# Kernel tuning notes

Measured on AMD Instinct MI355X. Metric: run time of the kernel, lower is better.

Reference implementation:

```python
import jax, jax.numpy as jnp
import numpy as np

B, S, D, H, E = 2, 512, 768, 12, 8
FF = 4 * D
HD = D // H


def setup_inputs() -> dict:
    key = jax.random.key(0)
    ks = jax.random.split(key, 12)
    s = 0.02
    return {
        "x": jax.random.normal(ks[0], (B, S, D), jnp.float32),
        "ln1_g": jnp.ones((D,), jnp.float32),
        "ln1_b": jnp.zeros((D,), jnp.float32),
        "ln2_g": jnp.ones((D,), jnp.float32),
        "ln2_b": jnp.zeros((D,), jnp.float32),
        "in_proj_w": jax.random.normal(ks[1], (3 * D, D), jnp.float32) * s,
        "in_proj_b": jax.random.normal(ks[2], (3 * D,), jnp.float32) * s,
        "out_proj_w": jax.random.normal(ks[3], (D, D), jnp.float32) * s,
        "out_proj_b": jax.random.normal(ks[4], (D,), jnp.float32) * s,
        "router_w": jax.random.normal(ks[5], (E, D), jnp.float32) * s,
        "router_b": jax.random.normal(ks[6], (E,), jnp.float32) * s,
        "w1": jax.random.normal(ks[7], (E, D, FF), jnp.float32) * s,
        "b1": jax.random.normal(ks[8], (E, FF), jnp.float32) * s,
        "w2": jax.random.normal(ks[9], (E, FF, D), jnp.float32) * s,
        "b2": jax.random.normal(ks[10], (E, D), jnp.float32) * s,
    }


def _layernorm(x, g, b, eps=1e-5):
    mu = x.mean(-1, keepdims=True)
    var = ((x - mu) ** 2).mean(-1, keepdims=True)
    return (x - mu) * jax.lax.rsqrt(var + eps) * g + b


def _forward(x, ln1_g, ln1_b, ln2_g, ln2_b, in_proj_w, in_proj_b,
             out_proj_w, out_proj_b, router_w, router_b, w1, b1, w2, b2):
    # --- self-attention sublayer (pre-norm per torch module ordering) ---
    h = _layernorm(x, ln1_g, ln1_b)
    qkv = h @ in_proj_w.T + in_proj_b                     # [B,S,3D]
    q, k, v = jnp.split(qkv, 3, axis=-1)
    to_heads = lambda t: t.reshape(B, S, H, HD).transpose(0, 2, 1, 3)  # [B,H,S,hd]
    q, k, v = to_heads(q), to_heads(k), to_heads(v)
    scores = jnp.einsum('bhqd,bhkd->bhqk', q, k) / np.float32(np.sqrt(HD))
    attn = jax.nn.softmax(scores, axis=-1)
    o = jnp.einsum('bhqk,bhkd->bhqd', attn, v).transpose(0, 2, 1, 3).reshape(B, S, D)
    o = o @ out_proj_w.T + out_proj_b
    x = x + o
    # --- MoE sublayer: top-2 routing, renormalized gates ---
    h2 = _layernorm(x, ln2_g, ln2_b)
    t = h2.reshape(-1, D)                                  # [T,D]
    logits = t @ router_w.T + router_b                     # [T,E]
    probs = jax.nn.softmax(logits, axis=-1)
    top_v, top_i = jax.lax.top_k(probs, 2)                 # [T,2]
    top_v = top_v / top_v.sum(-1, keepdims=True)
    # per-(token, expert) combine weight (0 if expert not in token's top-2)
    comb = jnp.sum(jax.nn.one_hot(top_i, E, dtype=probs.dtype) * top_v[..., None], axis=1)  # [T,E]
    # dense grouped-FFN: every token through every expert, zero-weighted combine
    hid = jax.nn.gelu(jnp.einsum('td,edf->tef', t, w1) + b1, approximate=False)  # exact GELU as torch
    y = jnp.einsum('tef,efd->ted', hid, w2) + b2           # [T,E,D]
    moe = jnp.einsum('te,ted->td', comb, y).reshape(B, S, D)
    return x + moe


def reference(x, ln1_g, ln1_b, ln2_g, ln2_b, in_proj_w, in_proj_b,
              out_proj_w, out_proj_b, router_w, router_b, w1, b1, w2, b2):
    return _forward(x, ln1_g, ln1_b, ln2_g, ln2_b, in_proj_w, in_proj_b,
                    out_proj_w, out_proj_b, router_w, router_b, w1, b1, w2, b2)
```

## Files before the change

### kernel.cpp

```cpp
#include <hip/hip_runtime.h>
#include <hip/hip_bf16.h>

#define BATCH 2
#define SEQ 512
#define DIM 768
#define HEADS 12
#define NEXP 8
#define FFDIM 3072
#define HDIM 64
#define NTOK (BATCH*SEQ)
#define NENT (2*NTOK)

typedef __hip_bfloat16 bf16;
typedef __attribute__((ext_vector_type(8))) short s8v;
typedef __attribute__((ext_vector_type(4))) float f4v;

typedef __attribute__((address_space(1))) const unsigned char gas_u8;
typedef __attribute__((address_space(3))) unsigned char las_u8;
__device__ __forceinline__ void gload16(const void* g, void* l) {
    __builtin_amdgcn_global_load_lds((gas_u8*)g, (las_u8*)l, 16, 0, 0);
}

__global__ __launch_bounds__(256) void ln_kernel(const float* __restrict__ x,
                                                 const float* __restrict__ g,
                                                 const float* __restrict__ b,
                                                 float* __restrict__ outf,
                                                 bf16* __restrict__ outb) {
    int t = blockIdx.x;
    const float* xr = x + (long)t * DIM;
    int tid = threadIdx.x;
    float v0 = xr[tid], v1 = xr[tid + 256], v2 = xr[tid + 512];
    float s = v0 + v1 + v2;
    __shared__ float red[4];
    #pragma unroll
    for (int o = 32; o; o >>= 1) s += __shfl_xor(s, o);
    if ((tid & 63) == 0) red[tid >> 6] = s;
    __syncthreads();
    s = red[0] + red[1] + red[2] + red[3];
    float mu = s * (1.f / DIM);
    float d0 = v0 - mu, d1 = v1 - mu, d2 = v2 - mu;
    float q = d0*d0 + d1*d1 + d2*d2;
    __shared__ float red2[4];
    #pragma unroll
    for (int o = 32; o; o >>= 1) q += __shfl_xor(q, o);
    if ((tid & 63) == 0) red2[tid >> 6] = q;
    __syncthreads();
    q = red2[0] + red2[1] + red2[2] + red2[3];
    float rstd = rsqrtf(q * (1.f / DIM) + 1e-5f);
    float o0 = d0 * rstd * g[tid]       + b[tid];
    float o1 = d1 * rstd * g[tid + 256] + b[tid + 256];
    float o2 = d2 * rstd * g[tid + 512] + b[tid + 512];
    if (outf) {
        float* of = outf + (long)t * DIM;
        of[tid] = o0; of[tid + 256] = o1; of[tid + 512] = o2;
    }
    if (outb) {
        bf16* ob = outb + (long)t * DIM;
        ob[tid] = __float2bfloat16(o0);
        ob[tid + 256] = __float2bfloat16(o1);
        ob[tid + 512] = __float2bfloat16(o2);
    }
}

template<int WM, int WN, bool GROUPED, bool GELU, int OUTMODE>
__global__ __launch_bounds__(256) void mfma_gemm(
    const bf16* __restrict__ A, const bf16* __restrict__ B,
    const float* __restrict__ bias, const float* __restrict__ resid,
    void* __restrict__ Cv,
    int M, int N, int K, int lda, int ldb, int ldc,
    int zdiv, int ksplit,
    long a_hi, long a_lo, long b_hi, long b_lo, long c_hi, long c_lo,
    long bias_stride, const int* __restrict__ grp_off, float alpha)
{
    constexpr int BM = 32 * WM, BN = 32 * WN;
    constexpr int ACH = BM * 4;
    constexpr int BCH = BN * 4;

    int z = blockIdx.z;
    int ze = z / ksplit, ks = z % ksplit;
    int kper = K / ksplit;
    long aoff, boff, coff;
    int m_count = M;
    if (GROUPED) {
        int m0 = grp_off[ze], m1 = grp_off[ze + 1];
        m_count = m1 - m0;
        if ((int)blockIdx.y * BM >= m_count) return;
        aoff = (long)m0 * lda;
        coff = (long)m0 * ldc;
        boff = (long)ze * b_hi;
    } else {
        int zh = ze / zdiv, zl = ze % zdiv;
        aoff = zh * a_hi + zl * a_lo;
        boff = zh * b_hi + zl * b_lo;
        coff = zh * c_hi + zl * c_lo;
    }
    const short* Ag = (const short*)(A + aoff);
    const short* Bg = (const short*)(B + boff);
    const float* biasp = bias ? bias + (long)ze * bias_stride : nullptr;
    float* Cf = (float*)Cv + coff;
    bf16*  Cb = (bf16*)Cv + coff;

    __shared__ short As[BM * 32];
    __shared__ short Bs[BN * 32];

    int tid = threadIdx.x;
    int wv = tid >> 6, ln = tid & 63;
    int wr = wv >> 1, wc = wv & 1;
    int fr = ln & 15, fq = ln >> 4;
    int bm = blockIdx.y * BM, bn = blockIdx.x * BN;

    f4v acc[WM][WN] = {};

    for (int k0 = ks * kper; k0 < (ks + 1) * kper; k0 += 32) {
        #pragma unroll
        for (int is = 0; is < ACH / 256; ++is) {
            int c = is * 256 + wv * 64 + ln;
            int m = c >> 2, kq = c & 3;
            gload16(Ag + (long)(bm + m) * lda + k0 + kq * 8,
                    &As[(is * 256 + wv * 64) * 8]);
        }
        if constexpr (ACH % 256) {
            if (tid < ACH % 256) {
                int c = (ACH / 256) * 256 + tid;
                int m = c >> 2, kq = c & 3;
                gload16(Ag + (long)(bm + m) * lda + k0 + kq * 8,
                        &As[((ACH / 256) * 256 + wv * 64) * 8]);
            }
        }
        #pragma unroll
        for (int is = 0; is < BCH / 256; ++is) {
            int c = is * 256 + wv * 64 + ln;
            int m = c >> 2, kq = c & 3;
            gload16(Bg + (long)(bn + m) * ldb + k0 + kq * 8,
                    &Bs[(is * 256 + wv * 64) * 8]);
        }
        if constexpr (BCH % 256) {
            if (tid < BCH % 256) {
                int c = (BCH / 256) * 256 + tid;
                int m = c >> 2, kq = c & 3;
                gload16(Bg + (long)(bn + m) * ldb + k0 + kq * 8,
                        &Bs[((BCH / 256) * 256 + wv * 64) * 8]);
            }
        }
        __syncthreads();
        s8v av[WM], bv[WN];
        #pragma unroll
        for (int i = 0; i < WM; ++i)
            av[i] = *(const s8v*)&As[(wr * (WM * 16) + i * 16 + fr) * 32 + fq * 8];
        #pragma unroll
        for (int j = 0; j < WN; ++j)
            bv[j] = *(const s8v*)&Bs[(wc * (WN * 16) + j * 16 + fr) * 32 + fq * 8];
        #pragma unroll
        for (int i = 0; i < WM; ++i)
            #pragma unroll
            for (int j = 0; j < WN; ++j)
                acc[i][j] = __builtin_amdgcn_mfma_f32_16x16x32_bf16(av[i], bv[j], acc[i][j], 0, 0, 0);
        __syncthreads();
    }

    #pragma unroll
    for (int i = 0; i < WM; ++i) {
        #pragma unroll
        for (int r = 0; r < 4; ++r) {
            int row = bm + wr * (WM * 16) + i * 16 + fq * 4 + r;
            if (GROUPED && row >= m_count) continue;
            #pragma unroll
            for (int j = 0; j < WN; ++j) {
                int col = bn + wc * (WN * 16) + j * 16 + fr;
                if (col < N) {
                    float v = acc[i][j][r] * alpha;
                    if (OUTMODE == 2) {
                        atomicAdd(&Cf[(long)row * ldc + col], v);
                    } else {
                        if (biasp) v += biasp[col];
                        if (GELU) v = 0.5f * v * (1.f + erff(v * 0.70710678118654752f));
                        if (resid) v += resid[(long)row * ldc + col];
                        if (OUTMODE == 1) Cb[(long)row * ldc + col] = __float2bfloat16(v);
                        else              Cf[(long)row * ldc + col] = v;
                    }
                }
            }
        }
    }
}

template<int FM, int FN, int XT, int YCAP, int KS, bool GELU, int OUTMODE>
__global__ __launch_bounds__(256) void moe_gemm(
    const bf16* __restrict__ A, const bf16* __restrict__ B,
    const float* __restrict__ bias, void* __restrict__ Cv,
    int lda, int ldb, int ldc, int Ktot, long b_hi, long bias_stride,
    const int* __restrict__ grp_off, int N)
{
    static_assert(OUTMODE != 1 || KS == 1, "plain store requires no split-K");
    constexpr int BM = FM * 32, BN = FN * 32;
    constexpr int GA = BM / 64;
    constexpr int GB = BN / 64;
    constexpr int G = GA + GB;

    int bid = blockIdx.x;
    int e = bid & 7;
    int r = bid >> 3;
    int xt = r % XT; r /= XT;
    int yt = r % YCAP;
    int ks = r / YCAP;
    int m0 = grp_off[e], m1 = grp_off[e + 1];
    int m_count = m1 - m0;
    int bm = yt * BM;
    if (bm >= m_count) return;
    int bn = xt * BN;
    int kper = Ktot / KS;

    const short* Ag = (const short*)A + (long)m0 * lda;
    const short* Bg = (const short*)(B + (long)e * b_hi);
    const float* biasp = bias ? bias + (long)e * bias_stride : nullptr;
    float* Cf = (float*)Cv + (long)m0 * ldc;
    bf16*  Cb = (bf16*)Cv + (long)m0 * ldc;

    __shared__ short As[3][BM * 32];
    __shared__ short Bs[3][BN * 32];

    int tid = threadIdx.x;
    int wv = tid >> 6, ln = tid & 63;
    int wr = wv >> 1, wc = wv & 1;
    int fr = ln & 15, fq = ln >> 4;

    f4v acc[FM][FN] = {};

    auto stage = [&](int buf, int k0) {
        #pragma unroll
        for (int is = 0; is < GA; ++is) {
            int c = is * 256 + wv * 64 + ln;
            int m = c >> 2, q = c & 3;
            int qg = q ^ ((m >> 1) & 3);
            gload16(Ag + (long)(bm + m) * lda + k0 + qg * 8,
                    &As[buf][(is * 256 + wv * 64) * 8]);
        }
        #pragma unroll
        for (int is = 0; is < GB; ++is) {
            int c = is * 256 + wv * 64 + ln;
            int n = c >> 2, q = c & 3;
            int qg = q ^ ((n >> 1) & 3);
            gload16(Bg + (long)(bn + n) * ldb + k0 + qg * 8,
                    &Bs[buf][(is * 256 + wv * 64) * 8]);
        }
    };

    int kbeg = ks * kper;
    int nit = kper / 32;
    stage(0, kbeg);
    if (nit > 1) stage(1, kbeg + 32);

    for (int it = 0; it < nit; ++it) {
        if (it + 1 < nit) asm volatile("s_waitcnt vmcnt(%0)" :: "i"(G) : "memory");
        else              asm volatile("s_waitcnt vmcnt(0)" ::: "memory");
        __builtin_amdgcn_s_barrier();
        if (it + 2 < nit) stage((it + 2) % 3, kbeg + (it + 2) * 32);
        int cur = it % 3;
        __builtin_amdgcn_s_setprio(1);
        {
            s8v av[FM], bv[FN];
            #pragma unroll
            for (int i = 0; i < FM; ++i) {
                int row = wr * (FM * 16) + i * 16 + fr;
                av[i] = *(const s8v*)&As[cur][row * 32 + (fq ^ ((row >> 1) & 3)) * 8];
            }
            #pragma unroll
            for (int j = 0; j < FN; ++j) {
                int row = wc * (FN * 16) + j * 16 + fr;
                bv[j] = *(const s8v*)&Bs[cur][row * 32 + (fq ^ ((row >> 1) & 3)) * 8];
            }
            #pragma unroll
            for (int i = 0; i < FM; ++i)
                #pragma unroll
                for (int j = 0; j < FN; ++j)
                    acc[i][j] = __builtin_amdgcn_mfma_f32_16x16x32_bf16(av[i], bv[j], acc[i][j], 0, 0, 0);
        }
        __builtin_amdgcn_s_setprio(0);
    }

    #pragma unroll
    for (int i = 0; i < FM; ++i) {
        #pragma unroll
        for (int rr = 0; rr < 4; ++rr) {
            int row = bm + wr * (FM * 16) + i * 16 + fq * 4 + rr;
            if (row >= m_count) continue;
            #pragma unroll
            for (int j = 0; j < FN; ++j) {
                int col = bn + wc * (FN * 16) + j * 16 + fr;
                float v = acc[i][j][rr];
                if (OUTMODE == 2) {
                    atomicAdd(&Cf[(long)row * ldc + col], v);
                } else {
                    if (biasp) v += biasp[col];
                    if (GELU) v = 0.5f * v * (1.f + erff(v * 0.70710678118654752f));
                    Cb[(long)row * ldc + col] = __float2bfloat16(v);
                }
            }
        }
    }
}

__global__ __launch_bounds__(256) void softmax512(const float* __restrict__ s,
                                                  bf16* __restrict__ attn) {
    long row = blockIdx.x;
    const float* p = s + row * 512;
    int tid = threadIdx.x;
    float a = p[tid], b = p[tid + 256];
    float m = fmaxf(a, b);
    __shared__ float red[4], red2[4];
    #pragma unroll
    for (int o = 32; o; o >>= 1) m = fmaxf(m, __shfl_xor(m, o));
    if ((tid & 63) == 0) red[tid >> 6] = m;
    __syncthreads();
    m = fmaxf(fmaxf(red[0], red[1]), fmaxf(red[2], red[3]));
    float e0 = expf(a - m), e1 = expf(b - m);
    float ssum = e0 + e1;
    #pragma unroll
    for (int o = 32; o; o >>= 1) ssum += __shfl_xor(ssum, o);
    if ((tid & 63) == 0) red2[tid >> 6] = ssum;
    __syncthreads();
    ssum = red2[0] + red2[1] + red2[2] + red2[3];
    float inv = 1.f / ssum;
    bf16* ar = attn + row * 512;
    ar[tid]       = __float2bfloat16(e0 * inv);
    ar[tid + 256] = __float2bfloat16(e1 * inv);
}

__global__ __launch_bounds__(256) void vt_kernel(const bf16* __restrict__ qkvb,
                                                 bf16* __restrict__ vt) {
    int st = blockIdx.x;
    int z = blockIdx.y;
    int b = z / HEADS, h = z % HEADS;
    __shared__ short tile[64][65];
    int t = threadIdx.x;
    int d = t & 63, s0 = t >> 6;
    const short* q = (const short*)qkvb;
    #pragma unroll
    for (int i = 0; i < 16; ++i) {
        int s = st * 64 + s0 + i * 4;
        tile[s0 + i * 4][d] = q[(long)(b * SEQ + s) * 2304 + 2 * DIM + h * HDIM + d];
    }
    __syncthreads();
    short* o = (short*)vt;
    #pragma unroll
    for (int i = 0; i < 16; ++i) {
        int d2 = (t >> 6) + i * 4;
        o[(long)(z * 64 + d2) * 512 + st * 64 + (t & 63)] = tile[t & 63][d2];
    }
}

__global__ __launch_bounds__(256) void wtrans_kernel(const float* __restrict__ in,
                                                     bf16* __restrict__ out,
                                                     int R, int C) {
    int z = blockIdx.z;
    long ibase = (long)z * R * C;
    int rt = blockIdx.y * 64, ct = blockIdx.x * 64;
    __shared__ float tile[64][65];
    int t = threadIdx.x;
    int c = t & 63, r0 = t >> 6;
    #pragma unroll
    for (int i = 0; i < 16; ++i)
        tile[r0 + i * 4][c] = in[ibase + (long)(rt + r0 + i * 4) * C + ct + c];
    __syncthreads();
    #pragma unroll
    for (int i = 0; i < 16; ++i) {
        int cc = r0 + i * 4;
        out[ibase + (long)(ct + cc) * R + rt + c] = __float2bfloat16(tile[c][cc]);
    }
}

__global__ __launch_bounds__(256) void cvt_kernel(const float* __restrict__ in,
                                                  bf16* __restrict__ out, long n) {
    long i = ((long)blockIdx.x * 256 + threadIdx.x) * 4;
    if (i >= n) return;
    float4 v = *(const float4*)(in + i);
    out[i]     = __float2bfloat16(v.x);
    out[i + 1] = __float2bfloat16(v.y);
    out[i + 2] = __float2bfloat16(v.z);
    out[i + 3] = __float2bfloat16(v.w);
}

__global__ __launch_bounds__(64) void router_kernel(const float* __restrict__ t2,
                                                    const float* __restrict__ rw,
                                                    const float* __restrict__ rb,
                                                    int* __restrict__ e_sel,
                                                    float* __restrict__ w_sel) {
    int t = blockIdx.x;
    int lane = threadIdx.x;
    const float* tr = t2 + (long)t * DIM;
    float tv[12];
    #pragma unroll
    for (int i = 0; i < 12; ++i) tv[i] = tr[lane + 64 * i];
    float logits[NEXP];
    #pragma unroll
    for (int e = 0; e < NEXP; ++e) {
        const float* wr = rw + (long)e * DIM;
        float s = 0.f;
        #pragma unroll
        for (int i = 0; i < 12; ++i) s += tv[i] * wr[lane + 64 * i];
        #pragma unroll
        for (int o = 32; o; o >>= 1) s += __shfl_xor(s, o);
        logits[e] = s + rb[e];
    }
    if (lane == 0) {
        int e0 = -1, e1 = -1;
        float l0 = -1e30f, l1 = -1e30f;
        #pragma unroll
        for (int e = 0; e < NEXP; ++e) {
            float l = logits[e];
            if (l > l0) { l1 = l0; e1 = e0; l0 = l; e0 = e; }
            else if (l > l1) { l1 = l; e1 = e; }
        }
        float p1 = expf(l1 - l0);
        float inv = 1.f / (1.f + p1);
        e_sel[t * 2] = e0;  e_sel[t * 2 + 1] = e1;
        w_sel[t * 2] = inv; w_sel[t * 2 + 1] = p1 * inv;
    }
}

__global__ __launch_bounds__(1024) void build_lists(const int* __restrict__ e_sel,
                                                    int* __restrict__ entry_tok,
                                                    int* __restrict__ ent_exp,
                                                    int* __restrict__ pos,
                                                    int* __restrict__ grp_off) {
    __shared__ int cnt[NEXP];
    __shared__ int off[NEXP + 1];
    __shared__ int cur[NEXP];
    int tid = threadIdx.x;
    if (tid < NEXP) cnt[tid] = 0;
    __syncthreads();
    for (int i = tid; i < NENT; i += 1024) atomicAdd(&cnt[e_sel[i]], 1);
    __syncthreads();
    if (tid == 0) {
        off[0] = 0;
        for (int e = 0; e < NEXP; ++e) off[e + 1] = off[e] + cnt[e];
        for (int e = 0; e < NEXP; ++e) cur[e] = off[e];
    }
    __syncthreads();
    for (int i = tid; i < NENT; i += 1024) {
        int e = e_sel[i];
        int p = atomicAdd(&cur[e], 1);
        entry_tok[p] = i >> 1;
        ent_exp[p] = e;
        pos[i] = p;
    }
    if (tid < NEXP + 1) grp_off[tid] = off[tid];
}

__global__ __launch_bounds__(256) void gather_kernel(const bf16* __restrict__ t2b,
                                                     const int* __restrict__ entry_tok,
                                                     bf16* __restrict__ t2g) {
    long i = (long)blockIdx.x * 256 + threadIdx.x;
    if (i >= (long)NENT * 192) return;
    int p = (int)(i / 192), q = (int)(i % 192);
    ((uint2*)t2g)[(long)p * 192 + q] = ((const uint2*)t2b)[(long)entry_tok[p] * 192 + q];
}

__global__ __launch_bounds__(256) void prefill_x1(const float* __restrict__ x,
                                                  const float* __restrict__ out_b,
                                                  float* __restrict__ x1) {
    long i = ((long)blockIdx.x * 256 + threadIdx.x) * 4;
    if (i >= (long)NTOK * DIM) return;
    int d = (int)(i % DIM);
    float4 v = *(const float4*)(x + i);
    v.x += out_b[d]; v.y += out_b[d + 1]; v.z += out_b[d + 2]; v.w += out_b[d + 3];
    *(float4*)(x1 + i) = v;
}

__global__ __launch_bounds__(256) void prefill_ybuf(const float* __restrict__ b2,
                                                    const int* __restrict__ ent_exp,
                                                    float* __restrict__ ybuf) {
    long i = ((long)blockIdx.x * 256 + threadIdx.x) * 4;
    if (i >= (long)NENT * DIM) return;
    int p = (int)(i / DIM), d = (int)(i % DIM);
    *(float4*)(ybuf + i) = *(const float4*)(b2 + (long)ent_exp[p] * DIM + d);
}

__global__ __launch_bounds__(256) void combine_kernel(const float* __restrict__ x1,
                                                      const float* __restrict__ ybuf,
                                                      const int* __restrict__ pos,
                                                      const float* __restrict__ wsel,
                                                      float* __restrict__ out) {
    long i = (long)blockIdx.x * 256 + threadIdx.x;
    if (i >= (long)NTOK * DIM) return;
    int t = (int)(i / DIM), d = (int)(i % DIM);
    float v = x1[i];
    v += wsel[t * 2]     * ybuf[(long)pos[t * 2]     * DIM + d];
    v += wsel[t * 2 + 1] * ybuf[(long)pos[t * 2 + 1] * DIM + d];
    out[i] = v;
}

extern "C" void kernel_launch(void* const* d_in, const int* in_sizes, int n_in,
                              void* d_out, int out_size, void* d_ws, size_t ws_size,
                              hipStream_t stream) {
    const float* x        = (const float*)d_in[0];
    const float* ln1_g    = (const float*)d_in[1];
    const float* ln1_b    = (const float*)d_in[2];
    const float* ln2_g    = (const float*)d_in[3];
    const float* ln2_b    = (const float*)d_in[4];
    const float* in_w     = (const float*)d_in[5];
    const float* in_b     = (const float*)d_in[6];
    const float* out_w    = (const float*)d_in[7];
    const float* out_b    = (const float*)d_in[8];
    const float* router_w = (const float*)d_in[9];
    const float* router_b = (const float*)d_in[10];
    const float* w1       = (const float*)d_in[11];
    const float* b1       = (const float*)d_in[12];
    const float* w2       = (const float*)d_in[13];
    const float* b2       = (const float*)d_in[14];
    float* out = (float*)d_out;

    const long TD = (long)NTOK * DIM;
    char* p = (char*)d_ws;
    size_t off = 0;
    auto alloc = [&](size_t bytes) -> void* {
        void* r = p + off; off += (bytes + 255) & ~(size_t)255; return r;
    };
    bf16*  h_b    = (bf16*)alloc(TD * 2);
    bf16*  in_wb  = (bf16*)alloc(2304L * 768 * 2);
    bf16*  qkv_b  = (bf16*)alloc(1024L * 2304 * 2);
    bf16*  out_wb = (bf16*)alloc(768L * 768 * 2);
    bf16*  vt_b   = (bf16*)alloc((24L * 64 + 64) * 512 * 2);
    bf16*  oat_b  = (bf16*)alloc(TD * 2);
    float* x1     = (float*)alloc(TD * 4);
    float* t2     = (float*)alloc(TD * 4);
    bf16*  t2b    = (bf16*)alloc(TD * 2);
    bf16*  t2g    = (bf16*)alloc((2048L + 256) * 768 * 2);
    bf16*  w1t    = (bf16*)alloc(8L * 3072 * 768 * 2);
    bf16*  w2t    = (bf16*)alloc(8L * 768 * 3072 * 2);
    bf16*  hid    = (bf16*)alloc((2048L + 256) * 3072 * 2);
    float* ybuf   = (float*)alloc(2048L * 768 * 4);
    int*   e_sel     = (int*)alloc(NENT * 4);
    float* w_sel     = (float*)alloc(NENT * 4);
    int*   entry_tok = (int*)alloc(NENT * 4);
    int*   ent_exp   = (int*)alloc(NENT * 4);
    int*   pos       = (int*)alloc(NENT * 4);
    int*   grp_off   = (int*)alloc(64);
    float* scores = (float*)w1t;
    bf16*  attn   = (bf16*)((char*)w1t + 24L * 512 * 512 * 4);

    ln_kernel<<<NTOK, 256, 0, stream>>>(x, ln1_g, ln1_b, nullptr, h_b);
    cvt_kernel<<<1728, 256, 0, stream>>>(in_w, in_wb, 2304L * 768);
    cvt_kernel<<<576, 256, 0, stream>>>(out_w, out_wb, 768L * 768);
    mfma_gemm<2, 2, false, false, 1><<<dim3(36, 16, 1), 256, 0, stream>>>(
        h_b, in_wb, in_b, nullptr, qkv_b,
        NTOK, 3 * DIM, DIM, DIM, DIM, 3 * DIM,
        1, 1, 0, 0, 0, 0, 0, 0, 0, nullptr, 1.f);
    mfma_gemm<2, 4, false, false, 0><<<dim3(4, 8, 24), 256, 0, stream>>>(
        qkv_b, qkv_b + DIM, nullptr, nullptr, scores,
        SEQ, SEQ, HDIM, 3 * DIM, 3 * DIM, SEQ,
        HEADS, 1, (long)SEQ * 3 * DIM, HDIM, (long)SEQ * 3 * DIM, HDIM,
        (long)HEADS * SEQ * SEQ, (long)SEQ * SEQ,
        0, nullptr, 0.125f);
    softmax512<<<24 * SEQ, 256, 0, stream>>>(scores, attn);
    vt_kernel<<<dim3(8, 24), 256, 0, stream>>>(qkv_b, vt_b);
    mfma_gemm<1, 2, false, false, 1><<<dim3(1, 16, 24), 256, 0, stream>>>(
        attn, vt_b, nullptr, nullptr, oat_b,
        SEQ, HDIM, SEQ, SEQ, SEQ, DIM,
        HEADS, 1, (long)HEADS * SEQ * SEQ, (long)SEQ * SEQ,
        (long)HEADS * HDIM * SEQ, (long)HDIM * SEQ,
        (long)SEQ * DIM, HDIM,
        0, nullptr, 1.f);
    prefill_x1<<<768, 256, 0, stream>>>(x, out_b, x1);
    mfma_gemm<2, 2, false, false, 2><<<dim3(12, 16, 2), 256, 0, stream>>>(
        oat_b, out_wb, nullptr, nullptr, x1,
        NTOK, DIM, DIM, DIM, DIM, DIM,
        1, 2, 0, 0, 0, 0, 0, 0, 0, nullptr, 1.f);
    ln_kernel<<<NTOK, 256, 0, stream>>>(x1, ln2_g, ln2_b, t2, t2b);
    router_kernel<<<NTOK, 64, 0, stream>>>(t2, router_w, router_b, e_sel, w_sel);
    build_lists<<<1, 1024, 0, stream>>>(e_sel, entry_tok, ent_exp, pos, grp_off);
    gather_kernel<<<1536, 256, 0, stream>>>(t2b, entry_tok, t2g);
    wtrans_kernel<<<dim3(48, 12, 8), 256, 0, stream>>>(w1, w1t, DIM, FFDIM);
    moe_gemm<4, 4, 24, 8, 1, true, 1><<<8 * 24 * 8, 256, 0, stream>>>(
        t2g, w1t, b1, hid,
        DIM, DIM, FFDIM, DIM, (long)FFDIM * DIM, FFDIM, grp_off, FFDIM);
    wtrans_kernel<<<dim3(12, 48, 8), 256, 0, stream>>>(w2, w2t, FFDIM, DIM);
    prefill_ybuf<<<1536, 256, 0, stream>>>(b2, ent_exp, ybuf);
    moe_gemm<4, 4, 6, 8, 4, false, 2><<<8 * 6 * 8 * 4, 256, 0, stream>>>(
        hid, w2t, nullptr, ybuf,
        FFDIM, FFDIM, DIM, FFDIM, (long)DIM * FFDIM, 0, grp_off, DIM);
    combine_kernel<<<3072, 256, 0, stream>>>(x1, ybuf, pos, w_sel, out);
}
```

Before: 213.1 us.

## Store attention scores in bf16, wave-per-row softmax, merge weight casts, retile MoE GEMMs

The QK^T GEMM now writes its scores as bf16 instead of fp32, which halves the score traffic. A new softmax has one wavefront handle each row with 16-byte vector loads and stores and no LDS barriers. The two weight fp32-to-bf16 cast launches are merged into one kernel. Both MoE GEMMs switch from 128x128 tiles to 256x64 tiles with twice as many column tiles, and the GA/GB load-group constants are rewritten as a byte-based formula that gives the same values. Rounding scores to bf16 before softmax adds precision risk, and the new tile shape changes register pressure and weight reuse.

```diff
diff --git a/kernel.cpp b/kernel.cpp
--- a/kernel.cpp
+++ b/kernel.cpp
@@ -19,6 +19,10 @@
 typedef __attribute__((address_space(3))) unsigned char las_u8;
 __device__ __forceinline__ void gload16(const void* g, void* l) {
     __builtin_amdgcn_global_load_lds((gas_u8*)g, (las_u8*)l, 16, 0, 0);
+}
+
+__device__ __forceinline__ float bfbits2f(unsigned hi16) {
+    union { unsigned u; float f; } c; c.u = hi16; return c.f;
 }
 
 __global__ __launch_bounds__(256) void ln_kernel(const float* __restrict__ x,
@@ -193,8 +197,8 @@
 {
     static_assert(OUTMODE != 1 || KS == 1, "plain store requires no split-K");
     constexpr int BM = FM * 32, BN = FN * 32;
-    constexpr int GA = BM / 64;
-    constexpr int GB = BN / 64;
+    constexpr int GA = (BM * 32 * 2) / 4096;
+    constexpr int GB = (BN * 32 * 2) / 4096;
     constexpr int G = GA + GB;
 
     int bid = blockIdx.x;
@@ -300,30 +304,39 @@
     }
 }
 
-__global__ __launch_bounds__(256) void softmax512(const float* __restrict__ s,
-                                                  bf16* __restrict__ attn) {
-    long row = blockIdx.x;
-    const float* p = s + row * 512;
-    int tid = threadIdx.x;
-    float a = p[tid], b = p[tid + 256];
-    float m = fmaxf(a, b);
-    __shared__ float red[4], red2[4];
+__global__ __launch_bounds__(256) void softmax512b(const bf16* __restrict__ s,
+                                                   bf16* __restrict__ attn) {
+    long row = (long)blockIdx.x * 4 + (threadIdx.x >> 6);
+    int ln = threadIdx.x & 63;
+    const unsigned* p = (const unsigned*)(s + row * 512);
+    uint4 v = *(const uint4*)(p + ln * 4);
+    unsigned u[4] = {v.x, v.y, v.z, v.w};
+    float f[8];
+    #pragma unroll
+    for (int j = 0; j < 4; ++j) {
+        f[2*j]   = bfbits2f(u[j] << 16);
+        f[2*j+1] = bfbits2f(u[j] & 0xffff0000u);
+    }
+    float m = f[0];
+    #pragma unroll
+    for (int j = 1; j < 8; ++j) m = fmaxf(m, f[j]);
     #pragma unroll
     for (int o = 32; o; o >>= 1) m = fmaxf(m, __shfl_xor(m, o));
-    if ((tid & 63) == 0) red[tid >> 6] = m;
-    __syncthreads();
-    m = fmaxf(fmaxf(red[0], red[1]), fmaxf(red[2], red[3]));
-    float e0 = expf(a - m), e1 = expf(b - m);
-    float ssum = e0 + e1;
+    float e[8], ssum = 0.f;
+    #pragma unroll
+    for (int j = 0; j < 8; ++j) { e[j] = expf(f[j] - m); ssum += e[j]; }
     #pragma unroll
     for (int o = 32; o; o >>= 1) ssum += __shfl_xor(ssum, o);
-    if ((tid & 63) == 0) red2[tid >> 6] = ssum;
-    __syncthreads();
-    ssum = red2[0] + red2[1] + red2[2] + red2[3];
     float inv = 1.f / ssum;
-    bf16* ar = attn + row * 512;
-    ar[tid]       = __float2bfloat16(e0 * inv);
-    ar[tid + 256] = __float2bfloat16(e1 * inv);
+    unsigned w[4];
+    #pragma unroll
+    for (int j = 0; j < 4; ++j) {
+        bf16 lo = __float2bfloat16(e[2*j] * inv);
+        bf16 hi = __float2bfloat16(e[2*j+1] * inv);
+        w[j] = ((unsigned)*(unsigned short*)&hi << 16) | *(unsigned short*)&lo;
+    }
+    uint4 o4; o4.x = w[0]; o4.y = w[1]; o4.z = w[2]; o4.w = w[3];
+    *(uint4*)((unsigned*)(attn + row * 512) + ln * 4) = o4;
 }
 
 __global__ __launch_bounds__(256) void vt_kernel(const bf16* __restrict__ qkvb,
@@ -369,15 +382,20 @@
     }
 }
 
-__global__ __launch_bounds__(256) void cvt_kernel(const float* __restrict__ in,
-                                                  bf16* __restrict__ out, long n) {
+__global__ __launch_bounds__(256) void cvt2_kernel(const float* __restrict__ a, long na,
+                                                   const float* __restrict__ b, long nb,
+                                                   bf16* __restrict__ oa,
+                                                   bf16* __restrict__ ob) {
     long i = ((long)blockIdx.x * 256 + threadIdx.x) * 4;
-    if (i >= n) return;
-    float4 v = *(const float4*)(in + i);
-    out[i]     = __float2bfloat16(v.x);
-    out[i + 1] = __float2bfloat16(v.y);
-    out[i + 2] = __float2bfloat16(v.z);
-    out[i + 3] = __float2bfloat16(v.w);
+    const float* src; bf16* dst; long idx;
+    if (i < na) { src = a; dst = oa; idx = i; }
+    else if (i < na + nb) { src = b; dst = ob; idx = i - na; }
+    else return;
+    float4 v = *(const float4*)(src + idx);
+    dst[idx]     = __float2bfloat16(v.x);
+    dst[idx + 1] = __float2bfloat16(v.y);
+    dst[idx + 2] = __float2bfloat16(v.z);
+    dst[idx + 3] = __float2bfloat16(v.w);
 }
 
 __global__ __launch_bounds__(64) void router_kernel(const float* __restrict__ t2,
@@ -536,23 +554,23 @@
     int*   ent_exp   = (int*)alloc(NENT * 4);
     int*   pos       = (int*)alloc(NENT * 4);
     int*   grp_off   = (int*)alloc(64);
-    float* scores = (float*)w1t;
-    bf16*  attn   = (bf16*)((char*)w1t + 24L * 512 * 512 * 4);
+    bf16* scores = w1t;
+    bf16* attn   = (bf16*)((char*)w1t + 24L * 512 * 512 * 2);
 
     ln_kernel<<<NTOK, 256, 0, stream>>>(x, ln1_g, ln1_b, nullptr, h_b);
-    cvt_kernel<<<1728, 256, 0, stream>>>(in_w, in_wb, 2304L * 768);
-    cvt_kernel<<<576, 256, 0, stream>>>(out_w, out_wb, 768L * 768);
+    cvt2_kernel<<<2304, 256, 0, stream>>>(in_w, 2304L * 768, out_w, 768L * 768,
+                                          in_wb, out_wb);
     mfma_gemm<2, 2, false, false, 1><<<dim3(36, 16, 1), 256, 0, stream>>>(
         h_b, in_wb, in_b, nullptr, qkv_b,
         NTOK, 3 * DIM, DIM, DIM, DIM, 3 * DIM,
         1, 1, 0, 0, 0, 0, 0, 0, 0, nullptr, 1.f);
-    mfma_gemm<2, 4, false, false, 0><<<dim3(4, 8, 24), 256, 0, stream>>>(
+    mfma_gemm<2, 4, false, false, 1><<<dim3(4, 8, 24), 256, 0, stream>>>(
         qkv_b, qkv_b + DIM, nullptr, nullptr, scores,
         SEQ, SEQ, HDIM, 3 * DIM, 3 * DIM, SEQ,
         HEADS, 1, (long)SEQ * 3 * DIM, HDIM, (long)SEQ * 3 * DIM, HDIM,
         (long)HEADS * SEQ * SEQ, (long)SEQ * SEQ,
         0, nullptr, 0.125f);
-    softmax512<<<24 * SEQ, 256, 0, stream>>>(scores, attn);
+    softmax512b<<<24 * SEQ / 4, 256, 0, stream>>>(scores, attn);
     vt_kernel<<<dim3(8, 24), 256, 0, stream>>>(qkv_b, vt_b);
     mfma_gemm<1, 2, false, false, 1><<<dim3(1, 16, 24), 256, 0, stream>>>(
         attn, vt_b, nullptr, nullptr, oat_b,
@@ -571,12 +589,12 @@
     build_lists<<<1, 1024, 0, stream>>>(e_sel, entry_tok, ent_exp, pos, grp_off);
     gather_kernel<<<1536, 256, 0, stream>>>(t2b, entry_tok, t2g);
     wtrans_kernel<<<dim3(48, 12, 8), 256, 0, stream>>>(w1, w1t, DIM, FFDIM);
-    moe_gemm<4, 4, 24, 8, 1, true, 1><<<8 * 24 * 8, 256, 0, stream>>>(
+    moe_gemm<8, 2, 48, 8, 1, true, 1><<<8 * 48 * 8, 256, 0, stream>>>(
         t2g, w1t, b1, hid,
         DIM, DIM, FFDIM, DIM, (long)FFDIM * DIM, FFDIM, grp_off, FFDIM);
     wtrans_kernel<<<dim3(12, 48, 8), 256, 0, stream>>>(w2, w2t, FFDIM, DIM);
     prefill_ybuf<<<1536, 256, 0, stream>>>(b2, ent_exp, ybuf);
-    moe_gemm<4, 4, 6, 8, 4, false, 2><<<8 * 6 * 8 * 4, 256, 0, stream>>>(
+    moe_gemm<8, 2, 12, 8, 4, false, 2><<<8 * 12 * 8 * 4, 256, 0, stream>>>(
         hid, w2t, nullptr, ybuf,
         FFDIM, FFDIM, DIM, FFDIM, (long)DIM * FFDIM, 0, grp_off, DIM);
     combine_kernel<<<3072, 256, 0, stream>>>(x1, ybuf, pos, w_sel, out);
```

New measurement: 243.7 us. 14.4% more time.
